# Kernel tuning notes

Measured on AMD Instinct MI355X. Metric: run time of the kernel, lower is better.

The kernel has to match this reference:

```python
import jax, jax.numpy as jnp
import numpy as np

P, G, F, H = 128, 256, 1024, 512
EPS = 1e-5

def _bn(x, g, b, m, v):
    # eval-mode BatchNorm1d over last dim
    return (x - m) / jnp.sqrt(v + EPS) * g + b

def _lrelu(x):
    return jnp.where(x > 0, x, 0.1 * x)

def setup_inputs():
    key = jax.random.key(0)
    ks = iter(jax.random.split(key, 64))
    rn = lambda s, sc=1.0: jax.random.normal(next(ks), s, dtype=jnp.float32) * sc
    ru = lambda s: jax.random.uniform(next(ks), s, dtype=jnp.float32) + 0.5
    return {
        "f_p": rn((P, F)), "f_g": rn((G, F)),
        "bn_g": ru((F,)), "bn_b": rn((F,), 0.1), "bn_m": rn((F,), 0.1), "bn_v": ru((F,)),
        "rf_W1": rn((F, F), 0.02), "rf_b1": rn((F,), 0.01),
        "rf1_g": ru((F,)), "rf1_b": rn((F,), 0.1), "rf1_m": rn((F,), 0.1), "rf1_v": ru((F,)),
        "rf_W2": rn((F, F), 0.02), "rf_b2": rn((F,), 0.01),
        "rf2_g": ru((F,)), "rf2_b": rn((F,), 0.1), "rf2_m": rn((F,), 0.1), "rf2_v": ru((F,)),
        "sfc_W": rn((F, H), 0.02), "sfc_b": rn((H,), 0.01),
        "sbn_g": ru((H,)), "sbn_b": rn((H,), 0.1), "sbn_m": rn((H,), 0.1), "sbn_v": ru((H,)),
        "scl_W": rn((H, 1), 0.001), "scl_b": rn((1,), 0.001),
        "ffc_W": rn((F, H), 0.02), "ffc_b": rn((H,), 0.01),
        "fbn_g": ru((H,)), "fbn_b": rn((H,), 0.1), "fbn_m": rn((H,), 0.1), "fbn_v": ru((H,)),
        "cls_W": rn((H, 1), 0.001), "cls_b": rn((1,), 0.001),
    }

def reference(f_p, f_g, bn_g, bn_b, bn_m, bn_v,
              rf_W1, rf_b1, rf1_g, rf1_b, rf1_m, rf1_v,
              rf_W2, rf_b2, rf2_g, rf2_b, rf2_m, rf2_v,
              sfc_W, sfc_b, sbn_g, sbn_b, sbn_m, sbn_v, scl_W, scl_b,
              ffc_W, ffc_b, fbn_g, fbn_b, fbn_m, fbn_v, cls_W, cls_b):
    # Siamese difference feature for every probe-gallery pair: d [P,G,F]
    d = _bn((f_p[:, None, :] - f_g[None, :, :]) ** 2, bn_g, bn_b, bn_m, bn_v)
    h = _lrelu(_bn(d @ rf_W1 + rf_b1, rf1_g, rf1_b, rf1_m, rf1_v))
    t = _lrelu(_bn(h @ rf_W2 + rf_b2, rf2_g, rf2_b, rf2_m, rf2_v))
    # Gallery-gallery scalar affinities via Siamese FcBlock + ClassBlock: w [G,G]
    dg = _bn((f_g[:, None, :] - f_g[None, :, :]) ** 2, bn_g, bn_b, bn_m, bn_v)
    hg = _lrelu(_bn(dg @ sfc_W + sfc_b, sbn_g, sbn_b, sbn_m, sbn_v))
    w = (hg @ scl_W + scl_b)[..., 0]
    # Graph diffusion over the gallery axis: d_new = t @ w  [P,G,F]
    d_new = jnp.einsum('pgf,gh->phf', t, w)
    # Per-pair FC + classifier -> scalar score per (probe, gallery) pair
    feat = _lrelu(_bn(d_new @ ffc_W + ffc_b, fbn_g, fbn_b, fbn_m, fbn_v))
    result = (feat @ cls_W + cls_b)[..., 0]
    return result
```

## Files before the change

### kernel.cpp

```cpp
#include <hip/hip_runtime.h>


typedef __bf16 bf16;
typedef __attribute__((ext_vector_type(8))) __bf16 bf16x8;
typedef __attribute__((ext_vector_type(4))) float f32x4;

#define EPSV 1e-5f

__device__ __forceinline__ void async_load16(const bf16* g, bf16* l) {
    __builtin_amdgcn_global_load_lds(
        (const __attribute__((address_space(1))) void*)g,
        (__attribute__((address_space(3))) void*)l, 16, 0, 0);
}

__global__ __launch_bounds__(256) void prep_kernel(
    const float* __restrict__ g, const float* __restrict__ b,
    const float* __restrict__ m, const float* __restrict__ v,
    const float* __restrict__ bias, float* __restrict__ scale,
    float* __restrict__ offset, int n)
{
    int i = blockIdx.x * 256 + threadIdx.x;
    if (i >= n) return;
    float s = g[i] / sqrtf(v[i] + EPSV);
    float o = b[i] - m[i] * s;
    if (bias) o += bias[i] * s;
    scale[i] = s;
    offset[i] = o;
}

__global__ __launch_bounds__(256) void wtrans_kernel(
    const float* __restrict__ in, bf16* __restrict__ out, int K, int N)
{
    int k = blockIdx.x * 256 + threadIdx.x;
    int n = blockIdx.y;
    out[(size_t)n * K + k] = (bf16)in[(size_t)k * N + n];
}

__global__ __launch_bounds__(256) void wconv_kernel(
    const float* __restrict__ w_acc, const float* __restrict__ sclb,
    bf16* __restrict__ wT)
{
    int tid = blockIdx.x * 256 + threadIdx.x;
    int g2 = tid >> 8, g1 = tid & 255;
    int idx = ((g1 >> 4) <= (g2 >> 4)) ? (g1 * 256 + g2) : (g2 * 256 + g1);
    wT[tid] = (bf16)(w_acc[idx] + sclb[0]);
}

__global__ __launch_bounds__(256) void finout_kernel(
    const float* __restrict__ acc, const float* __restrict__ clsb,
    float* __restrict__ out)
{
    int i = blockIdx.x * 256 + threadIdx.x;
    out[i] = acc[i] + clsb[0];
}

__global__ __launch_bounds__(256) void dprep_kernel(
    const float* __restrict__ X, const float* __restrict__ Y,
    const float* __restrict__ ps, const float* __restrict__ po,
    bf16* __restrict__ d, int rowOff)
{
    int t  = blockIdx.x * 256 + threadIdx.x;
    int k0 = (t & 127) * 8;
    int r  = t >> 7;
    int gr = rowOff + r;
    const float* xp = X + (size_t)(gr >> 8) * 1024 + k0;
    const float* yp = Y + (size_t)(gr & 255) * 1024 + k0;
    f32x4 x0 = *(const f32x4*)xp, x1 = *(const f32x4*)(xp + 4);
    f32x4 y0 = *(const f32x4*)yp, y1 = *(const f32x4*)(yp + 4);
    f32x4 sa = *(const f32x4*)(ps + k0), sb = *(const f32x4*)(ps + k0 + 4);
    f32x4 oa = *(const f32x4*)(po + k0), ob = *(const f32x4*)(po + k0 + 4);
    bf16x8 dv;
#pragma unroll
    for (int j = 0; j < 4; ++j) {
        float d0 = x0[j] - y0[j];
        float d1 = x1[j] - y1[j];
        dv[j]     = (bf16)(d0 * d0 * sa[j] + oa[j]);
        dv[j + 4] = (bf16)(d1 * d1 * sb[j] + ob[j]);
    }
    *(bf16x8*)&d[(size_t)r * 1024 + k0] = dv;
}

#define PHASE(ASB, BSB, Q, READB, STAGE_STMT, VM_STMT)                        \
  {                                                                           \
    if (READB) {                                                              \
      _Pragma("unroll") for (int ni = 0; ni < 4; ++ni) {                      \
        int rc = wcol * 64 + ni * 16 + l16;                                   \
        bfr[ni][0] = *(const bf16x8*)&(BSB)[rc * 64 + (((q) ^ (rc & 7)) * 8)];\
        bfr[ni][1] = *(const bf16x8*)&(BSB)[rc * 64 + (((4 + q) ^ (rc & 7)) * 8)];\
      }                                                                       \
    }                                                                         \
    bf16x8 afq[2][2];                                                         \
    _Pragma("unroll") for (int m2 = 0; m2 < 2; ++m2) {                        \
      int r = wrow * 128 + ((Q) * 2 + m2) * 16 + l16;                         \
      afq[m2][0] = *(const bf16x8*)&(ASB)[r * 64 + (((q) ^ (r & 7)) * 8)];    \
      afq[m2][1] = *(const bf16x8*)&(ASB)[r * 64 + (((4 + q) ^ (r & 7)) * 8)];\
    }                                                                         \
    STAGE_STMT;                                                               \
    VM_STMT;                                                                  \
    __builtin_amdgcn_s_barrier();                                             \
    asm volatile("s_waitcnt lgkmcnt(0)" ::: "memory");                        \
    __builtin_amdgcn_s_setprio(1);                                            \
    _Pragma("unroll") for (int s = 0; s < 2; ++s)                             \
      _Pragma("unroll") for (int m2 = 0; m2 < 2; ++m2)                        \
        _Pragma("unroll") for (int ni = 0; ni < 4; ++ni)                      \
          acc[(Q) * 2 + m2][ni] = __builtin_amdgcn_mfma_f32_16x16x32_bf16(    \
              afq[m2][s], bfr[ni][s], acc[(Q) * 2 + m2][ni], 0, 0, 0);        \
    __builtin_amdgcn_s_setprio(0);                                            \
    __builtin_amdgcn_s_barrier();                                             \
  }

__global__ __launch_bounds__(512) void gemm256(
    const bf16* __restrict__ A,
    const bf16* __restrict__ BT,
    bf16* __restrict__ C,
    int K, int N,
    long long batchA, long long batchB, long long batchC,
    const float* __restrict__ scale, const float* __restrict__ offset,
    int lrelu,
    const float* __restrict__ fuseW, float* __restrict__ facc,
    long long faccStride)
{
    __shared__ bf16 As[2 * 256 * 64];
    __shared__ bf16 Bs[2 * 256 * 64];
    const int tid  = threadIdx.x;
    const int lane = tid & 63;
    const int wave = tid >> 6;
    const int wrow = wave >> 2, wcol = wave & 3;
    const int q = lane >> 4, l16 = lane & 15;
    const int z = blockIdx.z;

    int bx = blockIdx.x, by = blockIdx.y;
    {
        int nwg = gridDim.x * gridDim.y;
        if (gridDim.z == 1 && (nwg & 7) == 0) {
            int lin = by * gridDim.x + bx;
            int cpx = nwg >> 3;
            int s = (lin & 7) * cpx + (lin >> 3);
            bx = s % gridDim.x;
            by = s / gridDim.x;
        }
    }
    const int row0 = by * 256;
    const int col0 = bx * 256;

    const bf16* Ap = A + (size_t)z * (size_t)batchA;
    const bf16* Bp = BT + (size_t)z * (size_t)batchB;

    f32x4 acc[8][4];
#pragma unroll
    for (int mi = 0; mi < 8; ++mi)
#pragma unroll
        for (int ni = 0; ni < 4; ++ni)
#pragma unroll
            for (int e = 0; e < 4; ++e) acc[mi][ni][e] = 0.f;

    auto stageA2 = [&](int kk, int buf, int h) {
#pragma unroll
        for (int tt = 0; tt < 2; ++tt) {
            int idx = (2 * h + tt) * 512 + tid;
            int r = idx >> 3, sch = idx & 7;
            int gch = sch ^ (r & 7);
            async_load16(Ap + (size_t)(row0 + r) * K + kk + gch * 8,
                         &As[buf * 16384 + idx * 8]);
        }
    };
    auto stageB2 = [&](int kk, int buf, int h) {
#pragma unroll
        for (int tt = 0; tt < 2; ++tt) {
            int idx = (2 * h + tt) * 512 + tid;
            int r = idx >> 3, sch = idx & 7;
            int gch = sch ^ (r & 7);
            async_load16(Bp + (size_t)(col0 + r) * K + kk + gch * 8,
                         &Bs[buf * 16384 + idx * 8]);
        }
    };

    stageA2(0, 0, 0); stageA2(0, 0, 1);
    stageB2(0, 0, 0); stageB2(0, 0, 1);
    stageB2(64, 1, 0); stageB2(64, 1, 1);
    asm volatile("s_waitcnt vmcnt(4)" ::: "memory");
    __builtin_amdgcn_s_barrier();

    bf16x8 bfr[4][2];
    const bf16* A0 = As;          const bf16* B0 = Bs;
    const bf16* A1 = As + 16384;  const bf16* B1 = Bs + 16384;
    const int nt = K >> 6;
    for (int i2 = 0; i2 < nt; i2 += 2) {
        const int kk1 = (i2 + 1) << 6, kk2 = (i2 + 2) << 6,
                  kk3 = (i2 + 3) << 6;
        const bool more = (i2 + 2) < nt;
        PHASE(A0, B0, 0, true,  { stageA2(kk1, 1, 0); }, {});
        PHASE(A0, B0, 1, false, { stageA2(kk1, 1, 1); }, {});
        PHASE(A0, B0, 2, false, { if (more) stageB2(kk2, 0, 0); }, {});
        PHASE(A0, B0, 3, false, { if (more) stageB2(kk2, 0, 1); },
              { if (more)
                    asm volatile("s_waitcnt vmcnt(4)" ::: "memory");
                else
                    asm volatile("s_waitcnt vmcnt(0)" ::: "memory"); });
        PHASE(A1, B1, 0, true,  { if (more) stageA2(kk2, 0, 0); }, {});
        PHASE(A1, B1, 1, false, { if (more) stageA2(kk2, 0, 1); }, {});
        PHASE(A1, B1, 2, false, { if (more) stageB2(kk3, 1, 0); }, {});
        PHASE(A1, B1, 3, false, { if (more) stageB2(kk3, 1, 1); },
              { if (more)
                    asm volatile("s_waitcnt vmcnt(4)" ::: "memory"); });
    }

    if (fuseW) {
#pragma unroll
        for (int mi = 0; mi < 8; ++mi)
#pragma unroll
            for (int i = 0; i < 4; ++i) {
                float rs = 0.f;
#pragma unroll
                for (int ni = 0; ni < 4; ++ni) {
                    int cc = col0 + wcol * 64 + ni * 16 + l16;
                    float val = acc[mi][ni][i] * scale[cc] + offset[cc];
                    val = val > 0.f ? val : 0.1f * val;
                    rs += val * fuseW[cc];
                }
                rs += __shfl_xor(rs, 1, 64);
                rs += __shfl_xor(rs, 2, 64);
                rs += __shfl_xor(rs, 4, 64);
                rs += __shfl_xor(rs, 8, 64);
                if (l16 == 0) {
                    int r = row0 + wrow * 128 + mi * 16 + q * 4 + i;
                    atomicAdd(facc + (size_t)z * faccStride + r, rs);
                }
            }
        return;
    }
    bf16* Cp = C + (size_t)z * (size_t)batchC;
#pragma unroll
    for (int mi = 0; mi < 8; ++mi)
#pragma unroll
        for (int ni = 0; ni < 4; ++ni)
#pragma unroll
            for (int i = 0; i < 4; ++i) {
                int r = row0 + wrow * 128 + mi * 16 + q * 4 + i;
                int cc = col0 + wcol * 64 + ni * 16 + l16;
                float val = acc[mi][ni][i];
                if (scale) val = val * scale[cc] + offset[cc];
                if (lrelu) val = val > 0.f ? val : 0.1f * val;
                Cp[(size_t)r * N + cc] = (bf16)val;
            }
}

__global__ __launch_bounds__(512) void gemm_aff(
    const float* __restrict__ pairX,
    const float* __restrict__ ps, const float* __restrict__ po,
    const bf16* __restrict__ BT,
    int K,
    const float* __restrict__ scale, const float* __restrict__ offset,
    const float* __restrict__ sclW, float* __restrict__ w_acc)
{
    __shared__ bf16 As[256 * 64];
    __shared__ bf16 Bs[128 * 64];
    const int tid  = threadIdx.x;
    const int lane = tid & 63;
    const int wave = tid >> 6;
    const int wrow = wave >> 1, wcol = wave & 1;
    const int q = lane >> 4, l16 = lane & 15;
    const int col0 = blockIdx.x * 128;

    int ta = 0, rem = blockIdx.y;
    while (rem >= 16 - ta) { rem -= 16 - ta; ++ta; }
    const int tb = ta + rem;

    f32x4 acc[4][4];
#pragma unroll
    for (int mi = 0; mi < 4; ++mi)
#pragma unroll
        for (int ni = 0; ni < 4; ++ni)
#pragma unroll
            for (int e = 0; e < 4; ++e) acc[mi][ni][e] = 0.f;

    for (int kk = 0; kk < K; kk += 64) {
#pragma unroll
        for (int t = 0; t < 4; ++t) {
            int c = tid + t * 512;
            int r = c >> 3, ch = c & 7;
            int g1 = ta * 16 + (r >> 4), g2 = tb * 16 + (r & 15);
            const float* xp = pairX + (size_t)g1 * K + kk + ch * 8;
            const float* yp = pairX + (size_t)g2 * K + kk + ch * 8;
            f32x4 x0 = *(const f32x4*)xp, x1 = *(const f32x4*)(xp + 4);
            f32x4 y0 = *(const f32x4*)yp, y1 = *(const f32x4*)(yp + 4);
            f32x4 sa = *(const f32x4*)(ps + kk + ch * 8);
            f32x4 sb = *(const f32x4*)(ps + kk + ch * 8 + 4);
            f32x4 oa = *(const f32x4*)(po + kk + ch * 8);
            f32x4 ob = *(const f32x4*)(po + kk + ch * 8 + 4);
            bf16x8 dv;
#pragma unroll
            for (int j = 0; j < 4; ++j) {
                float d0 = x0[j] - y0[j];
                float d1 = x1[j] - y1[j];
                dv[j]     = (bf16)(d0 * d0 * sa[j] + oa[j]);
                dv[j + 4] = (bf16)(d1 * d1 * sb[j] + ob[j]);
            }
            *(bf16x8*)&As[r * 64 + ((ch ^ (r & 7)) * 8)] = dv;
        }
#pragma unroll
        for (int t = 0; t < 2; ++t) {
            int idx = t * 512 + tid;
            int r = idx >> 3, sch = idx & 7;
            int gch = sch ^ (r & 7);
            async_load16(BT + (size_t)(col0 + r) * K + kk + gch * 8,
                         &Bs[idx * 8]);
        }
        __syncthreads();

#pragma unroll
        for (int s = 0; s < 2; ++s) {
            bf16x8 af[4], bfr[4];
#pragma unroll
            for (int mi = 0; mi < 4; ++mi) {
                int r = wrow * 64 + mi * 16 + l16;
                af[mi] = *(const bf16x8*)&As[r * 64 + (((s * 4 + q) ^ (r & 7)) * 8)];
            }
#pragma unroll
            for (int ni = 0; ni < 4; ++ni) {
                int rc = wcol * 64 + ni * 16 + l16;
                bfr[ni] = *(const bf16x8*)&Bs[rc * 64 + (((s * 4 + q) ^ (rc & 7)) * 8)];
            }
#pragma unroll
            for (int mi = 0; mi < 4; ++mi)
#pragma unroll
                for (int ni = 0; ni < 4; ++ni)
                    acc[mi][ni] = __builtin_amdgcn_mfma_f32_16x16x32_bf16(
                        af[mi], bfr[ni], acc[mi][ni], 0, 0, 0);
        }
        __syncthreads();
    }

#pragma unroll
    for (int mi = 0; mi < 4; ++mi)
#pragma unroll
        for (int i = 0; i < 4; ++i) {
            float rs = 0.f;
#pragma unroll
            for (int ni = 0; ni < 4; ++ni) {
                int cc = col0 + wcol * 64 + ni * 16 + l16;
                float val = acc[mi][ni][i] * scale[cc] + offset[cc];
                val = val > 0.f ? val : 0.1f * val;
                rs += val * sclW[cc];
            }
            rs += __shfl_xor(rs, 1, 64);
            rs += __shfl_xor(rs, 2, 64);
            rs += __shfl_xor(rs, 4, 64);
            rs += __shfl_xor(rs, 8, 64);
            if (l16 == 0) {
                int r = wrow * 64 + mi * 16 + q * 4 + i;
                int g1 = ta * 16 + (r >> 4), g2 = tb * 16 + (r & 15);
                atomicAdd(w_acc + g1 * 256 + g2, rs);
            }
        }
}

extern "C" void kernel_launch(void* const* d_in, const int* in_sizes, int n_in,
                              void* d_out, int out_size, void* d_ws, size_t ws_size,
                              hipStream_t stream)
{
    const float* f_p   = (const float*)d_in[0];
    const float* f_g   = (const float*)d_in[1];
    const float* bn_g  = (const float*)d_in[2];
    const float* bn_b  = (const float*)d_in[3];
    const float* bn_m  = (const float*)d_in[4];
    const float* bn_v  = (const float*)d_in[5];
    const float* rf_W1 = (const float*)d_in[6];
    const float* rf_b1 = (const float*)d_in[7];
    const float* rf1_g = (const float*)d_in[8];
    const float* rf1_b = (const float*)d_in[9];
    const float* rf1_m = (const float*)d_in[10];
    const float* rf1_v = (const float*)d_in[11];
    const float* rf_W2 = (const float*)d_in[12];
    const float* rf_b2 = (const float*)d_in[13];
    const float* rf2_g = (const float*)d_in[14];
    const float* rf2_b = (const float*)d_in[15];
    const float* rf2_m = (const float*)d_in[16];
    const float* rf2_v = (const float*)d_in[17];
    const float* sfc_W = (const float*)d_in[18];
    const float* sfc_b = (const float*)d_in[19];
    const float* sbn_g = (const float*)d_in[20];
    const float* sbn_b = (const float*)d_in[21];
    const float* sbn_m = (const float*)d_in[22];
    const float* sbn_v = (const float*)d_in[23];
    const float* scl_W = (const float*)d_in[24];
    const float* scl_b = (const float*)d_in[25];
    const float* ffc_W = (const float*)d_in[26];
    const float* ffc_b = (const float*)d_in[27];
    const float* fbn_g = (const float*)d_in[28];
    const float* fbn_b = (const float*)d_in[29];
    const float* fbn_m = (const float*)d_in[30];
    const float* fbn_v = (const float*)d_in[31];
    const float* cls_W = (const float*)d_in[32];
    const float* cls_b = (const float*)d_in[33];

    const size_t MB = 1ull << 20;
    char* ws = (char*)d_ws;
    float* SC      = (float*)(ws);
    float *s0 = SC,        *o0 = SC + 1024;
    float *s1 = SC + 2048, *o1 = SC + 3072;
    float *s2 = SC + 4096, *o2 = SC + 5120;
    float *s3 = SC + 6144, *o3 = SC + 6656;
    float *s4 = SC + 7168, *o4 = SC + 7680;
    float* w_acc   = (float*)(ws + 65536);
    float* out_acc = (float*)(ws + 327680);
    bf16* wT       = (bf16*)(ws + 458752);
    bf16* W1T      = (bf16*)(ws + 1 * MB);
    bf16* W2T      = (bf16*)(ws + 3 * MB);
    bf16* sfcT     = (bf16*)(ws + 5 * MB);
    bf16* ffcT     = (bf16*)(ws + 6 * MB);

    int nc;
    if      (ws_size >= 170 * MB) nc = 1;
    else if (ws_size >= 90 * MB)  nc = 2;
    else                          nc = 4;
    const int pc = 128 / nc;
    const int R  = pc * 256;
    const size_t hbytes = (size_t)R * 1024 * 2;
    bf16* bufA = (bf16*)(ws + 8 * MB);
    bf16* bufB = (bf16*)(ws + 8 * MB + hbytes);
    bf16* bufC = (bf16*)(ws + 8 * MB + 2 * hbytes);

    prep_kernel<<<dim3(4), 256, 0, stream>>>(bn_g, bn_b, bn_m, bn_v, nullptr, s0, o0, 1024);
    prep_kernel<<<dim3(4), 256, 0, stream>>>(rf1_g, rf1_b, rf1_m, rf1_v, rf_b1, s1, o1, 1024);
    prep_kernel<<<dim3(4), 256, 0, stream>>>(rf2_g, rf2_b, rf2_m, rf2_v, rf_b2, s2, o2, 1024);
    prep_kernel<<<dim3(2), 256, 0, stream>>>(sbn_g, sbn_b, sbn_m, sbn_v, sfc_b, s3, o3, 512);
    prep_kernel<<<dim3(2), 256, 0, stream>>>(fbn_g, fbn_b, fbn_m, fbn_v, ffc_b, s4, o4, 512);

    wtrans_kernel<<<dim3(4, 1024), 256, 0, stream>>>(rf_W1, W1T, 1024, 1024);
    wtrans_kernel<<<dim3(4, 1024), 256, 0, stream>>>(rf_W2, W2T, 1024, 1024);
    wtrans_kernel<<<dim3(4, 512), 256, 0, stream>>>(sfc_W, sfcT, 1024, 512);
    wtrans_kernel<<<dim3(4, 512), 256, 0, stream>>>(ffc_W, ffcT, 1024, 512);

    hipMemsetAsync(ws + 65536, 0, 393216, stream);

    gemm_aff<<<dim3(4, 136), 512, 0, stream>>>(
        f_g, s0, o0, sfcT, 1024, s3, o3, scl_W, w_acc);
    wconv_kernel<<<dim3(256), 256, 0, stream>>>(w_acc, scl_b, wT);

    for (int ci = 0; ci < nc; ++ci) {
        dprep_kernel<<<dim3(R / 2), 256, 0, stream>>>(
            f_p, f_g, s0, o0, bufB, ci * R);
        gemm256<<<dim3(4, R / 256), 512, 0, stream>>>(
            bufB, W1T, bufA, 1024, 1024,
            0, 0, 0, s1, o1, 1, nullptr, nullptr, 0);
        gemm256<<<dim3(4, R / 256), 512, 0, stream>>>(
            bufA, W2T, bufB, 1024, 1024,
            0, 0, 0, s2, o2, 1, nullptr, nullptr, 0);
        gemm256<<<dim3(1, 2, pc), 512, 0, stream>>>(
            ffcT, bufB, bufC, 1024, 256,
            0, (long long)256 * 1024, (long long)512 * 256,
            nullptr, nullptr, 0, nullptr, nullptr, 0);
        gemm256<<<dim3(2, 1, pc), 512, 0, stream>>>(
            wT, bufC, nullptr, 256, 512,
            0, (long long)512 * 256, 0,
            s4, o4, 1, cls_W, out_acc + (size_t)ci * pc * 256, 256);
    }
    finout_kernel<<<dim3(128), 256, 0, stream>>>(out_acc, cls_b, (float*)d_out);
}
```

Before: 520.9 us.

## Replace dedicated affinity GEMM with materialized pair diffs and tuned gemm256

Removes the simple single-buffered gemm_aff kernel, which built pair-difference tiles on the fly. The gallery-gallery pair differences are now written to a workspace buffer by a new prep kernel, which also records a row-to-(g1,g2) index map. The pipelined gemm256 then runs the FcBlock GEMM, scattering its fused classifier atomics through that map. This trades extra global memory traffic and a launch for the faster, double-buffered GEMM path.

```diff
diff --git a/kernel.cpp b/kernel.cpp
--- a/kernel.cpp
+++ b/kernel.cpp
@@ -78,6 +78,38 @@
         dv[j + 4] = (bf16)(d1 * d1 * sb[j] + ob[j]);
     }
     *(bf16x8*)&d[(size_t)r * 1024 + k0] = dv;
+}
+
+__global__ __launch_bounds__(256) void dgprep_kernel(
+    const float* __restrict__ X,
+    const float* __restrict__ ps, const float* __restrict__ po,
+    bf16* __restrict__ dg, int* __restrict__ affmap, int tileOff)
+{
+    int t  = blockIdx.x * 256 + threadIdx.x;
+    int k0 = (t & 127) * 8;
+    int r  = t >> 7;
+    int p  = tileOff + (r >> 8);
+    int ta = 0, rem = p;
+    while (rem >= 16 - ta) { rem -= 16 - ta; ++ta; }
+    int tb = ta + rem;
+    int rr = r & 255;
+    int g1 = ta * 16 + (rr >> 4), g2 = tb * 16 + (rr & 15);
+    const float* xp = X + (size_t)g1 * 1024 + k0;
+    const float* yp = X + (size_t)g2 * 1024 + k0;
+    f32x4 x0 = *(const f32x4*)xp, x1 = *(const f32x4*)(xp + 4);
+    f32x4 y0 = *(const f32x4*)yp, y1 = *(const f32x4*)(yp + 4);
+    f32x4 sa = *(const f32x4*)(ps + k0), sb = *(const f32x4*)(ps + k0 + 4);
+    f32x4 oa = *(const f32x4*)(po + k0), ob = *(const f32x4*)(po + k0 + 4);
+    bf16x8 dv;
+#pragma unroll
+    for (int j = 0; j < 4; ++j) {
+        float d0 = x0[j] - y0[j];
+        float d1 = x1[j] - y1[j];
+        dv[j]     = (bf16)(d0 * d0 * sa[j] + oa[j]);
+        dv[j + 4] = (bf16)(d1 * d1 * sb[j] + ob[j]);
+    }
+    *(bf16x8*)&dg[(size_t)r * 1024 + k0] = dv;
+    if (k0 == 0) affmap[r] = g1 * 256 + g2;
 }
 
 #define PHASE(ASB, BSB, Q, READB, STAGE_STMT, VM_STMT)                        \
@@ -118,7 +150,8 @@
     const float* __restrict__ scale, const float* __restrict__ offset,
     int lrelu,
     const float* __restrict__ fuseW, float* __restrict__ facc,
-    long long faccStride)
+    long long faccStride,
+    const int* __restrict__ affmap)
 {
     __shared__ bf16 As[2 * 256 * 64];
     __shared__ bf16 Bs[2 * 256 * 64];
@@ -224,7 +257,9 @@
                 rs += __shfl_xor(rs, 8, 64);
                 if (l16 == 0) {
                     int r = row0 + wrow * 128 + mi * 16 + q * 4 + i;
-                    atomicAdd(facc + (size_t)z * faccStride + r, rs);
+                    float* dst = affmap ? (facc + affmap[r])
+                                        : (facc + (size_t)z * faccStride + r);
+                    atomicAdd(dst, rs);
                 }
             }
         return;
@@ -243,116 +278,6 @@
                 if (lrelu) val = val > 0.f ? val : 0.1f * val;
                 Cp[(size_t)r * N + cc] = (bf16)val;
             }
-}
-
-__global__ __launch_bounds__(512) void gemm_aff(
-    const float* __restrict__ pairX,
-    const float* __restrict__ ps, const float* __restrict__ po,
-    const bf16* __restrict__ BT,
-    int K,
-    const float* __restrict__ scale, const float* __restrict__ offset,
-    const float* __restrict__ sclW, float* __restrict__ w_acc)
-{
-    __shared__ bf16 As[256 * 64];
-    __shared__ bf16 Bs[128 * 64];
-    const int tid  = threadIdx.x;
-    const int lane = tid & 63;
-    const int wave = tid >> 6;
-    const int wrow = wave >> 1, wcol = wave & 1;
-    const int q = lane >> 4, l16 = lane & 15;
-    const int col0 = blockIdx.x * 128;
-
-    int ta = 0, rem = blockIdx.y;
-    while (rem >= 16 - ta) { rem -= 16 - ta; ++ta; }
-    const int tb = ta + rem;
-
-    f32x4 acc[4][4];
-#pragma unroll
-    for (int mi = 0; mi < 4; ++mi)
-#pragma unroll
-        for (int ni = 0; ni < 4; ++ni)
-#pragma unroll
-            for (int e = 0; e < 4; ++e) acc[mi][ni][e] = 0.f;
-
-    for (int kk = 0; kk < K; kk += 64) {
-#pragma unroll
-        for (int t = 0; t < 4; ++t) {
-            int c = tid + t * 512;
-            int r = c >> 3, ch = c & 7;
-            int g1 = ta * 16 + (r >> 4), g2 = tb * 16 + (r & 15);
-            const float* xp = pairX + (size_t)g1 * K + kk + ch * 8;
-            const float* yp = pairX + (size_t)g2 * K + kk + ch * 8;
-            f32x4 x0 = *(const f32x4*)xp, x1 = *(const f32x4*)(xp + 4);
-            f32x4 y0 = *(const f32x4*)yp, y1 = *(const f32x4*)(yp + 4);
-            f32x4 sa = *(const f32x4*)(ps + kk + ch * 8);
-            f32x4 sb = *(const f32x4*)(ps + kk + ch * 8 + 4);
-            f32x4 oa = *(const f32x4*)(po + kk + ch * 8);
-            f32x4 ob = *(const f32x4*)(po + kk + ch * 8 + 4);
-            bf16x8 dv;
-#pragma unroll
-            for (int j = 0; j < 4; ++j) {
-                float d0 = x0[j] - y0[j];
-                float d1 = x1[j] - y1[j];
-                dv[j]     = (bf16)(d0 * d0 * sa[j] + oa[j]);
-                dv[j + 4] = (bf16)(d1 * d1 * sb[j] + ob[j]);
-            }
-            *(bf16x8*)&As[r * 64 + ((ch ^ (r & 7)) * 8)] = dv;
-        }
-#pragma unroll
-        for (int t = 0; t < 2; ++t) {
-            int idx = t * 512 + tid;
-            int r = idx >> 3, sch = idx & 7;
-            int gch = sch ^ (r & 7);
-            async_load16(BT + (size_t)(col0 + r) * K + kk + gch * 8,
-                         &Bs[idx * 8]);
-        }
-        __syncthreads();
-
-#pragma unroll
-        for (int s = 0; s < 2; ++s) {
-            bf16x8 af[4], bfr[4];
-#pragma unroll
-            for (int mi = 0; mi < 4; ++mi) {
-                int r = wrow * 64 + mi * 16 + l16;
-                af[mi] = *(const bf16x8*)&As[r * 64 + (((s * 4 + q) ^ (r & 7)) * 8)];
-            }
-#pragma unroll
-            for (int ni = 0; ni < 4; ++ni) {
-                int rc = wcol * 64 + ni * 16 + l16;
-                bfr[ni] = *(const bf16x8*)&Bs[rc * 64 + (((s * 4 + q) ^ (rc & 7)) * 8)];
-            }
-#pragma unroll
-            for (int mi = 0; mi < 4; ++mi)
-#pragma unroll
-                for (int ni = 0; ni < 4; ++ni)
-                    acc[mi][ni] = __builtin_amdgcn_mfma_f32_16x16x32_bf16(
-                        af[mi], bfr[ni], acc[mi][ni], 0, 0, 0);
-        }
-        __syncthreads();
-    }
-
-#pragma unroll
-    for (int mi = 0; mi < 4; ++mi)
-#pragma unroll
-        for (int i = 0; i < 4; ++i) {
-            float rs = 0.f;
-#pragma unroll
-            for (int ni = 0; ni < 4; ++ni) {
-                int cc = col0 + wcol * 64 + ni * 16 + l16;
-                float val = acc[mi][ni][i] * scale[cc] + offset[cc];
-                val = val > 0.f ? val : 0.1f * val;
-                rs += val * sclW[cc];
-            }
-            rs += __shfl_xor(rs, 1, 64);
-            rs += __shfl_xor(rs, 2, 64);
-            rs += __shfl_xor(rs, 4, 64);
-            rs += __shfl_xor(rs, 8, 64);
-            if (l16 == 0) {
-                int r = wrow * 64 + mi * 16 + q * 4 + i;
-                int g1 = ta * 16 + (r >> 4), g2 = tb * 16 + (r & 15);
-                atomicAdd(w_acc + g1 * 256 + g2, rs);
-            }
-        }
 }
 
 extern "C" void kernel_launch(void* const* d_in, const int* in_sizes, int n_in,
@@ -405,6 +330,7 @@
     float* w_acc   = (float*)(ws + 65536);
     float* out_acc = (float*)(ws + 327680);
     bf16* wT       = (bf16*)(ws + 458752);
+    int*  affmap   = (int*)(ws + 589824);
     bf16* W1T      = (bf16*)(ws + 1 * MB);
     bf16* W2T      = (bf16*)(ws + 3 * MB);
     bf16* sfcT     = (bf16*)(ws + 5 * MB);
@@ -434,8 +360,20 @@
 
     hipMemsetAsync(ws + 65536, 0, 393216, stream);
 
-    gemm_aff<<<dim3(4, 136), 512, 0, stream>>>(
-        f_g, s0, o0, sfcT, 1024, s3, o3, scl_W, w_acc);
+    {
+        bf16* dgc = (bf16*)(ws + 8 * MB);
+        const int na = (ws_size >= 170 * MB) ? 1 : 2;
+        const int TP = 136 / na;
+        for (int ai = 0; ai < na; ++ai) {
+            const int rows = TP * 256;
+            dgprep_kernel<<<dim3(rows / 2), 256, 0, stream>>>(
+                f_g, s0, o0, dgc, affmap + ai * TP * 256, ai * TP);
+            gemm256<<<dim3(2, rows / 256), 512, 0, stream>>>(
+                dgc, sfcT, nullptr, 1024, 512,
+                0, 0, 0, s3, o3, 1, scl_W, w_acc, 0,
+                affmap + ai * TP * 256);
+        }
+    }
     wconv_kernel<<<dim3(256), 256, 0, stream>>>(w_acc, scl_b, wT);
 
     for (int ci = 0; ci < nc; ++ci) {
@@ -443,18 +381,18 @@
             f_p, f_g, s0, o0, bufB, ci * R);
         gemm256<<<dim3(4, R / 256), 512, 0, stream>>>(
             bufB, W1T, bufA, 1024, 1024,
-            0, 0, 0, s1, o1, 1, nullptr, nullptr, 0);
+            0, 0, 0, s1, o1, 1, nullptr, nullptr, 0, nullptr);
         gemm256<<<dim3(4, R / 256), 512, 0, stream>>>(
             bufA, W2T, bufB, 1024, 1024,
-            0, 0, 0, s2, o2, 1, nullptr, nullptr, 0);
+            0, 0, 0, s2, o2, 1, nullptr, nullptr, 0, nullptr);
         gemm256<<<dim3(1, 2, pc), 512, 0, stream>>>(
             ffcT, bufB, bufC, 1024, 256,
             0, (long long)256 * 1024, (long long)512 * 256,
-            nullptr, nullptr, 0, nullptr, nullptr, 0);
+            nullptr, nullptr, 0, nullptr, nullptr, 0, nullptr);
         gemm256<<<dim3(2, 1, pc), 512, 0, stream>>>(
             wT, bufC, nullptr, 256, 512,
             0, (long long)512 * 256, 0,
-            s4, o4, 1, cls_W, out_acc + (size_t)ci * pc * 256, 256);
+            s4, o4, 1, cls_W, out_acc + (size_t)ci * pc * 256, 256, nullptr);
     }
     finout_kernel<<<dim3(128), 256, 0, stream>>>(out_acc, cls_b, (float*)d_out);
 }
```

Measured after the change: 523.3 us. About the same (+0.5%).
